# Optimization experiments

Hardware: AMD Instinct MI355X
Metric: run time of the kernel (lower is better)

The kernel has to match this reference:

```python
import jax, jax.numpy as jnp
import numpy as np

NUM_NODES_TARGET = 8000
MAX_CHILDREN = 64
BATCH = 2048
LABEL_SMOOTHING = 0.1


def _build_tree(seed=0):
    """Synthetic BFS hierarchy. Internal node ids are contiguous [0, num_internal)."""
    rng = np.random.RandomState(seed)
    parent = [-1]
    children = []  # children[i] = child ids of internal node i (BFS order)
    next_id = 1
    node = 0
    while node < next_id and NUM_NODES_TARGET - next_id >= 2:
        c = min(int(rng.randint(2, MAX_CHILDREN + 1)), NUM_NODES_TARGET - next_id)
        children.append(list(range(next_id, next_id + c)))
        parent.extend([node] * c)
        next_id += c
        node += 1
    num_nodes = next_id
    num_internal = len(children)
    cond_num = [len(ch) for ch in children]
    max_c = max(cond_num)
    row = np.concatenate([np.full(n, i, dtype=np.int64) for i, n in enumerate(cond_num)])
    col = np.concatenate([np.arange(n, dtype=np.int64) for n in cond_num])
    flat_index = row * max_c + col            # positions in padded [num_internal*max_c] buffer
    child_index = np.concatenate(children).astype(np.int64)  # = all non-root nodes
    parent = np.asarray(parent)
    leaves = np.arange(num_internal, num_nodes)
    L = len(leaves)
    # ancestor_mask[:, leaf_subset].T : mat[l, n] = 1 iff node n is ancestor-or-self of leaf l
    mat = np.zeros((L, num_nodes), np.float32)
    rows, cur = np.arange(L), leaves.copy()
    while cur.size:
        mat[rows, cur] = 1.0
        cur = parent[cur]
        keep = cur >= 0
        rows, cur = rows[keep], cur[keep]
    prior = (mat.sum(0) / np.float32(L)).astype(np.float32)  # hier.uniform_leaf
    return num_nodes, num_internal, max_c, flat_index, child_index, mat, prior


def setup_inputs() -> dict:
    num_nodes, num_internal, max_c, flat_index, child_index, mat, prior = _build_tree(0)
    key = jax.random.key(0)
    k1, k2 = jax.random.split(key)
    scores = jax.random.normal(k1, (BATCH, num_nodes - 1), dtype=jnp.float32)
    labels = jax.random.randint(k2, (BATCH,), 0, mat.shape[0])  # leaf label ids
    return {
        "scores": scores,
        "labels": labels,
        "matrix": jnp.asarray(mat),
        "prior": jnp.asarray(prior),
        "flat_index": jnp.asarray(flat_index),
        "child_index": jnp.asarray(child_index),
        "num_internal": num_internal,
        "max_num_children": max_c,
        "num_nodes": num_nodes,
    }


def reference(scores, labels, matrix, prior, flat_index, child_index,
              num_internal, max_num_children, num_nodes):
    B = scores.shape[0]
    # --- HierCondLogSoftmax: ragged softmax over each internal node's children,
    # padded to max_num_children with -inf (exp -> 0, so padding is inert).
    flat = jnp.full((B, num_internal * max_num_children), -jnp.inf, dtype=scores.dtype)
    flat = flat.at[:, flat_index].set(scores)
    child_log_p = jax.nn.log_softmax(
        flat.reshape(B, num_internal, max_num_children), axis=-1
    ).reshape(B, num_internal * max_num_children)
    # scatter per-child log-probs back to node order; root stays 0 (log 1)
    log_cond_p = jnp.zeros((B, num_nodes), dtype=scores.dtype)
    log_cond_p = log_cond_p.at[:, child_index].set(child_log_p[:, flat_index])
    # --- SumDescendants on one-hot leaf labels == row gather of ancestor matrix
    q = jnp.take(matrix, labels, axis=0)  # [B, num_nodes]
    q = (1.0 - LABEL_SMOOTHING) * q + LABEL_SMOOTHING * prior
    xent = jnp.sum(q * -log_cond_p, axis=-1)
    return jnp.mean(xent)
```

## Files before the change

### kernel.cpp

```cpp
#include <hip/hip_runtime.h>
#include <hip/hip_bf16.h>
#include <cstdint>


#define LSE_MAX 1024

__global__ __launch_bounds__(256) void hier_setup(
    const float* __restrict__ prior,
    const int* __restrict__ flat_index,
    const int* __restrict__ child_index,
    const int* __restrict__ p_max_c,
    int E,
    int* __restrict__ parent,
    int* __restrict__ gStart,
    int* __restrict__ gCount,
    float* __restrict__ priorSum)
{
    int j = blockIdx.x * 256 + threadIdx.x;
    if (j >= E) return;
    int mc  = *p_max_c;
    int fi  = flat_index[j];
    int row = fi / mc;
    int col = fi - row * mc;
    int node = child_index[j];
    parent[node] = row;
    if (col == 0) gStart[row] = j;
    atomicMax(&gCount[row], col + 1);
    atomicAdd(&priorSum[row], prior[node]);
}

__device__ __forceinline__ float lse_of_group(const float* s_sh, int st, int cnt) {
    float m = -INFINITY, ssum = 0.f;
    for (int t = 0; t < cnt; ++t) {
        float x = s_sh[st + t];
        if (x > m) { ssum = ssum * __expf(m - x) + 1.f; m = x; }
        else       { ssum += __expf(x - m); }
    }
    return m + __logf(ssum);
}

__global__ __launch_bounds__(256) void hier_main(
    const float* __restrict__ scores,
    const int* __restrict__ labels,
    const int* __restrict__ parent,
    const int* __restrict__ gStart,
    const int* __restrict__ gCount,
    const float* __restrict__ priorSum,
    const float* __restrict__ prior,
    const int* __restrict__ p_ni,
    int E,
    float* __restrict__ blockOut)
{
    __shared__ float s_sh[8000];
    __shared__ float lse_sh[LSE_MAX];
    __shared__ int   path_sh[64];
    __shared__ int   path_len_sh;
    __shared__ float red1[4];
    __shared__ float red2[4];

    const int b   = blockIdx.x;
    const int tid = threadIdx.x;
    const int NI  = *p_ni;

    if (tid == 0) {
        int cur = NI + labels[b];
        int d = 0;
        while (cur != 0 && d < 63) { path_sh[d++] = cur; cur = parent[cur]; }
        path_len_sh = d;
    }

    const float* rowp = scores + (size_t)b * (size_t)E;
    float t1 = 0.f;
    uintptr_t addr = (uintptr_t)rowp;
    int head = (int)(((16u - (unsigned)(addr & 15u)) & 15u) >> 2);
    if (head > E) head = E;
    for (int c = tid; c < head; c += 256) {
        float v = rowp[c]; s_sh[c] = v; t1 += v * prior[c + 1];
    }
    int nvec = (E - head) >> 2;
    const float4* row4 = (const float4*)(rowp + head);
    for (int v = tid; v < nvec; v += 256) {
        float4 x = row4[v];
        int c = head + v * 4;
        s_sh[c]     = x.x;
        s_sh[c + 1] = x.y;
        s_sh[c + 2] = x.z;
        s_sh[c + 3] = x.w;
        t1 += x.x * prior[c + 1] + x.y * prior[c + 2]
            + x.z * prior[c + 3] + x.w * prior[c + 4];
    }
    for (int c = head + nvec * 4 + tid; c < E; c += 256) {
        float v = rowp[c]; s_sh[c] = v; t1 += v * prior[c + 1];
    }

    __syncthreads();

    float t3a = 0.f;
    for (int i = tid; i < NI; i += 256) {
        float l = lse_of_group(s_sh, gStart[i], gCount[i]);
        if (i < LSE_MAX) lse_sh[i] = l;
        t3a += l * priorSum[i];
    }

    __syncthreads();

    for (int off = 32; off; off >>= 1) {
        t1  += __shfl_down(t1,  off);
        t3a += __shfl_down(t3a, off);
    }
    int wave = tid >> 6;
    if ((tid & 63) == 0) { red1[wave] = t1; red2[wave] = t3a; }
    __syncthreads();

    if (tid == 0) {
        float T1  = red1[0] + red1[1] + red1[2] + red1[3];
        float T3a = red2[0] + red2[1] + red2[2] + red2[3];
        float t2  = 0.f;
        float t3b = lse_sh[0];
        int d = path_len_sh;
        for (int k = 0; k < d; ++k) {
            int n = path_sh[k];
            t2 += s_sh[n - 1];
            if (k >= 1) {
                t3b += (n < LSE_MAX) ? lse_sh[n]
                                     : lse_of_group(s_sh, gStart[n], gCount[n]);
            }
        }
        blockOut[b] = -(0.1f * T1 + 0.9f * t2) + 0.1f * T3a + 0.9f * t3b;
    }
}

__global__ __launch_bounds__(256) void hier_reduce(
    const float* __restrict__ blockOut, int B, float* __restrict__ out)
{
    __shared__ double red[4];
    int tid = threadIdx.x;
    double s = 0.0;
    for (int i = tid; i < B; i += 256) s += (double)blockOut[i];
    for (int off = 32; off; off >>= 1) s += __shfl_down(s, off);
    if ((tid & 63) == 0) red[tid >> 6] = s;
    __syncthreads();
    if (tid == 0) out[0] = (float)((red[0] + red[1] + red[2] + red[3]) / (double)B);
}

extern "C" void kernel_launch(void* const* d_in, const int* in_sizes, int n_in,
                              void* d_out, int out_size, void* d_ws, size_t ws_size,
                              hipStream_t stream) {
    const float* scores      = (const float*)d_in[0];
    const int*   labels      = (const int*)  d_in[1];
    const float* prior       = (const float*)d_in[3];
    const int*   flat_index  = (const int*)  d_in[4];
    const int*   child_index = (const int*)  d_in[5];
    const int*   p_ni        = (const int*)  d_in[6];
    const int*   p_mc        = (const int*)  d_in[7];

    const int B = in_sizes[1];
    const int E = in_sizes[4];

    char* ws = (char*)d_ws;
    int*   parent   = (int*)  (ws);
    int*   gStart   = (int*)  (ws + 32768);
    int*   gCount   = (int*)  (ws + 49152);
    float* priorSum = (float*)(ws + 65536);
    float* blockOut = (float*)(ws + 81920);

    hipMemsetAsync(ws + 49152, 0, 32768, stream);

    hier_setup<<<(E + 255) / 256, 256, 0, stream>>>(
        prior, flat_index, child_index, p_mc, E, parent, gStart, gCount, priorSum);

    hier_main<<<B, 256, 0, stream>>>(
        scores, labels, parent, gStart, gCount, priorSum, prior, p_ni, E, blockOut);

    hier_reduce<<<1, 256, 0, stream>>>(blockOut, B, (float*)d_out);
}
```

Measured before the change: 365.7 us.

## Pre-shift prior into aligned copies and vectorize shared stores and prior loads

The setup kernel now writes four shifted copies of the prior so the main loop can read it as an aligned float4 matching the score row's misalignment, instead of doing four scalar unaligned loads. The shared score buffer is offset so float4 stores land aligned. The atomic max/add group metadata plus memset are replaced by the group-start thread scanning its own group sequentially. This adds workspace traffic and a serial per-group loop in setup, in exchange for fewer load instructions in the hot loop.

```diff
diff --git a/kernel.cpp b/kernel.cpp
--- a/kernel.cpp
+++ b/kernel.cpp
@@ -14,7 +14,9 @@
     int* __restrict__ parent,
     int* __restrict__ gStart,
     int* __restrict__ gCount,
-    float* __restrict__ priorSum)
+    float* __restrict__ priorSum,
+    float* __restrict__ P0, float* __restrict__ P1,
+    float* __restrict__ P2, float* __restrict__ P3)
 {
     int j = blockIdx.x * 256 + threadIdx.x;
     if (j >= E) return;
@@ -22,17 +24,31 @@
     int fi  = flat_index[j];
     int row = fi / mc;
     int col = fi - row * mc;
-    int node = child_index[j];
-    parent[node] = row;
-    if (col == 0) gStart[row] = j;
-    atomicMax(&gCount[row], col + 1);
-    atomicAdd(&priorSum[row], prior[node]);
+    parent[child_index[j]] = row;
+
+    P0[j] = prior[j + 1];
+    P1[j] = (j + 2 <= E) ? prior[j + 2] : 0.f;
+    P2[j] = (j + 3 <= E) ? prior[j + 3] : 0.f;
+    P3[j] = (j + 4 <= E) ? prior[j + 4] : 0.f;
+
+    if (col == 0) {
+        gStart[row] = j;
+        int lim = (row + 1) * mc;
+        float ps = prior[child_index[j]];
+        int cnt = 1;
+        while (j + cnt < E && flat_index[j + cnt] < lim) {
+            ps += prior[child_index[j + cnt]];
+            ++cnt;
+        }
+        gCount[row]   = cnt;
+        priorSum[row] = ps;
+    }
 }
 
-__device__ __forceinline__ float lse_of_group(const float* s_sh, int st, int cnt) {
+__device__ __forceinline__ float lse_of_group(const float* S, int st, int cnt) {
     float m = -INFINITY, ssum = 0.f;
     for (int t = 0; t < cnt; ++t) {
-        float x = s_sh[st + t];
+        float x = S[st + t];
         if (x > m) { ssum = ssum * __expf(m - x) + 1.f; m = x; }
         else       { ssum += __expf(x - m); }
     }
@@ -47,11 +63,13 @@
     const int* __restrict__ gCount,
     const float* __restrict__ priorSum,
     const float* __restrict__ prior,
+    const float* __restrict__ P0, const float* __restrict__ P1,
+    const float* __restrict__ P2, const float* __restrict__ P3,
     const int* __restrict__ p_ni,
     int E,
     float* __restrict__ blockOut)
 {
-    __shared__ float s_sh[8000];
+    __shared__ __align__(16) float s_sh[8008];
     __shared__ float lse_sh[LSE_MAX];
     __shared__ int   path_sh[64];
     __shared__ int   path_len_sh;
@@ -70,34 +88,35 @@
     }
 
     const float* rowp = scores + (size_t)b * (size_t)E;
-    float t1 = 0.f;
     uintptr_t addr = (uintptr_t)rowp;
     int head = (int)(((16u - (unsigned)(addr & 15u)) & 15u) >> 2);
     if (head > E) head = E;
+    const int pad = (4 - head) & 3;
+    float* S = s_sh + pad;
+    const float* Ph = (head == 0) ? P0 : (head == 1) ? P1 : (head == 2) ? P2 : P3;
+
+    float t1 = 0.f;
     for (int c = tid; c < head; c += 256) {
-        float v = rowp[c]; s_sh[c] = v; t1 += v * prior[c + 1];
+        float v = rowp[c]; S[c] = v; t1 += v * prior[c + 1];
     }
     int nvec = (E - head) >> 2;
     const float4* row4 = (const float4*)(rowp + head);
     for (int v = tid; v < nvec; v += 256) {
         float4 x = row4[v];
         int c = head + v * 4;
-        s_sh[c]     = x.x;
-        s_sh[c + 1] = x.y;
-        s_sh[c + 2] = x.z;
-        s_sh[c + 3] = x.w;
-        t1 += x.x * prior[c + 1] + x.y * prior[c + 2]
-            + x.z * prior[c + 3] + x.w * prior[c + 4];
+        *(float4*)(S + c) = x;
+        float4 p = *(const float4*)(Ph + (c - head));
+        t1 += x.x * p.x + x.y * p.y + x.z * p.z + x.w * p.w;
     }
     for (int c = head + nvec * 4 + tid; c < E; c += 256) {
-        float v = rowp[c]; s_sh[c] = v; t1 += v * prior[c + 1];
+        float v = rowp[c]; S[c] = v; t1 += v * prior[c + 1];
     }
 
     __syncthreads();
 
     float t3a = 0.f;
     for (int i = tid; i < NI; i += 256) {
-        float l = lse_of_group(s_sh, gStart[i], gCount[i]);
+        float l = lse_of_group(S, gStart[i], gCount[i]);
         if (i < LSE_MAX) lse_sh[i] = l;
         t3a += l * priorSum[i];
     }
@@ -120,10 +139,10 @@
         int d = path_len_sh;
         for (int k = 0; k < d; ++k) {
             int n = path_sh[k];
-            t2 += s_sh[n - 1];
+            t2 += S[n - 1];
             if (k >= 1) {
                 t3b += (n < LSE_MAX) ? lse_sh[n]
-                                     : lse_of_group(s_sh, gStart[n], gCount[n]);
+                                     : lse_of_group(S, gStart[n], gCount[n]);
             }
         }
         blockOut[b] = -(0.1f * T1 + 0.9f * t2) + 0.1f * T3a + 0.9f * t3b;
@@ -160,17 +179,21 @@
     char* ws = (char*)d_ws;
     int*   parent   = (int*)  (ws);
     int*   gStart   = (int*)  (ws + 32768);
-    int*   gCount   = (int*)  (ws + 49152);
-    float* priorSum = (float*)(ws + 65536);
-    float* blockOut = (float*)(ws + 81920);
-
-    hipMemsetAsync(ws + 49152, 0, 32768, stream);
+    int*   gCount   = (int*)  (ws + 36864);
+    float* priorSum = (float*)(ws + 40960);
+    float* P0       = (float*)(ws + 49152);
+    float* P1       = (float*)(ws + 81920);
+    float* P2       = (float*)(ws + 114688);
+    float* P3       = (float*)(ws + 147456);
+    float* blockOut = (float*)(ws + 180224);
 
     hier_setup<<<(E + 255) / 256, 256, 0, stream>>>(
-        prior, flat_index, child_index, p_mc, E, parent, gStart, gCount, priorSum);
+        prior, flat_index, child_index, p_mc, E,
+        parent, gStart, gCount, priorSum, P0, P1, P2, P3);
 
     hier_main<<<B, 256, 0, stream>>>(
-        scores, labels, parent, gStart, gCount, priorSum, prior, p_ni, E, blockOut);
+        scores, labels, parent, gStart, gCount, priorSum, prior,
+        P0, P1, P2, P3, p_ni, E, blockOut);
 
     hier_reduce<<<1, 256, 0, stream>>>(blockOut, B, (float*)d_out);
 }
```

After: 357.1 us. -2.4%, faster.
